# Kernel tuning notes

Measured on AMD Instinct MI355X. Metric: run time of the kernel, lower is better.

The kernel has to match this reference:

```python
import jax, jax.numpy as jnp
import numpy as np

N_ELEMENTS = 64  # StructureElementLayer(n_elements=64)


def setup_inputs() -> dict:
    key = jax.random.key(0)
    k1, k2 = jax.random.split(key)
    # x: [N, C, T, V] skeleton sequence (batch, coord channels, time, joints)
    x = jax.random.normal(k1, (256, 3, 256, 25), dtype=jnp.float32)
    # StructureElementLayer parameters (torch.rand init / ones*3 init)
    centres = jax.random.uniform(k2, (N_ELEMENTS, 2), dtype=jnp.float32)
    sharpness = jnp.ones((N_ELEMENTS, 2), dtype=jnp.float32) * 3.0
    return {"x": x, "centres": centres, "sharpness": sharpness}


def _mst_deaths(D):
    """Dim-0 Vietoris-Rips persistence deaths == MST edge weights (Prim's algorithm).

    D: [n, n] symmetric distance matrix. Returns [n-1] finite death values
    (births are all 0; the single essential (0, inf) pair contributes
    exp(-inf)=0 to the structure-element layer and is dropped).
    """
    n = D.shape[0]
    in_tree = jnp.zeros((n,), dtype=bool).at[0].set(True)
    dist = D[0]  # min distance from each node to the current tree

    def step(carry, _):
        in_tree, dist = carry
        d = jnp.where(in_tree, jnp.inf, dist)
        j = jnp.argmin(d)
        w = d[j]
        in_tree = in_tree.at[j].set(True)
        dist = jnp.minimum(dist, D[j])
        return (in_tree, dist), w

    (_, _), deaths = jax.lax.scan(step, (in_tree, dist), None, length=n - 1)
    return deaths


def _forward(x, centres, sharpness):
    xm = x.mean(1)                                  # [N, T, V]
    diff = xm[..., :, None] - xm[..., None, :]      # [N, T, V, V] pairwise joint diffs
    diff = diff.mean(-3)                            # [N, V, V]
    feat = jnp.linalg.norm(diff, axis=1)            # [N, V]  (torch.norm(., 2, dim=1))
    feat = (feat - feat.min()) / (feat.max() - feat.min())
    # Euclidean distance matrix of the N points in V-dim space (grad-safe sqrt)
    sq = jnp.sum(feat * feat, axis=1)
    D2 = sq[:, None] + sq[None, :] - 2.0 * (feat @ feat.T)
    D2 = jnp.maximum(D2, 0.0)
    D = jnp.where(D2 > 0.0, jnp.sqrt(jnp.where(D2 > 0.0, D2, 1.0)), 0.0)
    deaths = _mst_deaths(D)                         # [N-1]
    diag = jnp.stack([jnp.zeros_like(deaths), deaths], axis=-1)  # [N-1, 2] (birth, death)
    # StructureElementLayer: sum_i exp(-sum_d (p_id - c_kd)^2 * s_kd^2)
    d2 = (diag[:, None, :] - centres[None, :, :]) ** 2            # [N-1, K, 2]
    out = jnp.exp(-(d2 * (sharpness ** 2)).sum(-1)).sum(0)        # [K]
    return out


def reference(x, centres, sharpness):
    return _forward(x, centres, sharpness)
```

## Files before the change

kernel.cpp:

```cpp
#include <hip/hip_runtime.h>
#include <hip/hip_fp16.h>


#define WS_M    0
#define WS_MM   25600
#define WS_RK   28672
#define WS_DTH  29696
#define WS_NCDC 30720
#define WS_D16  65536
#define WS_MP   196608

#define INF32 0xFFFFFFFFu
#define MPSTR 132

__global__ void k_mean(const float* __restrict__ x, float* __restrict__ m,
                       unsigned int* __restrict__ Mp) {
    const int n = blockIdx.x;
    const int tid = threadIdx.x;
    if (tid < 66) Mp[n * 66 + tid] = INF32;
    __shared__ float sums[25];
    if (tid < 25) sums[tid] = 0.0f;
    __syncthreads();
    if (tid < 200) {
        const float* base = x + (long)n * 19200 + 4 * tid;
        float a0 = 0.f, a1 = 0.f, a2 = 0.f, a3 = 0.f;
        #pragma unroll
        for (int i = 0; i < 24; ++i) {
            float4 v = *reinterpret_cast<const float4*>(base + 800 * i);
            a0 += v.x; a1 += v.y; a2 += v.z; a3 += v.w;
        }
        const int v0 = (4 * tid) % 25;
        atomicAdd(&sums[v0], a0);
        atomicAdd(&sums[(v0 + 1) % 25], a1);
        atomicAdd(&sums[(v0 + 2) % 25], a2);
        atomicAdd(&sums[(v0 + 3) % 25], a3);
    }
    __syncthreads();
    if (tid < 25) m[n * 25 + tid] = sums[tid] * (1.0f / 768.0f);
}

template <int CTRL>
__device__ __forceinline__ unsigned int dpp_min_step(unsigned int v) {
    unsigned int t = (unsigned int)__builtin_amdgcn_update_dpp(
        (int)0xFFFFFFFF, (int)v, CTRL, 0xF, 0xF, false);
    return (t < v) ? t : v;
}

__global__ void __launch_bounds__(256) k_dist(const float* __restrict__ m,
                                              unsigned short* __restrict__ D16,
                                              unsigned int* __restrict__ rowKeyG,
                                              unsigned int* __restrict__ mm) {
    __shared__ float mS[6400];
    __shared__ float featS[6400];
    __shared__ unsigned int bmin, bmax;
    __shared__ unsigned int wred[4];
    const int i = blockIdx.x;
    const int t = threadIdx.x;
    if (t == 0) { bmin = 0x7F800000u; bmax = 0u; }
    #pragma unroll
    for (int it = 0; it < 7; ++it) {
        int o = it * 256 + t;
        if (o < 1600) reinterpret_cast<float4*>(mS)[o] =
            reinterpret_cast<const float4*>(m)[o];
    }
    __syncthreads();
    float r[25];
    #pragma unroll
    for (int v = 0; v < 25; ++v) r[v] = mS[t * 25 + v];
    float S1 = 0.f, S2 = 0.f;
    #pragma unroll
    for (int v = 0; v < 25; ++v) { S1 += r[v]; S2 += r[v] * r[v]; }
    float fmn = 1e30f, fmx = -1e30f;
    #pragma unroll
    for (int w = 0; w < 25; ++w) {
        float q = S2 - 2.f * r[w] * S1 + 25.f * r[w] * r[w];
        q = fmaxf(q, 0.f);
        float f = sqrtf(q);
        featS[t * 25 + w] = f;
        fmn = fminf(fmn, f); fmx = fmaxf(fmx, f);
    }
    if (i == 0) {
        atomicMin(&bmin, __float_as_uint(fmn));
        atomicMax(&bmax, __float_as_uint(fmx));
    }
    __syncthreads();
    if (i == 0 && t == 0) { mm[0] = bmin; mm[1] = bmax; }
    float fi[25];
    #pragma unroll
    for (int v = 0; v < 25; ++v) fi[v] = featS[i * 25 + v];
    float s = 0.f;
    #pragma unroll
    for (int v = 0; v < 25; ++v) { float d = fi[v] - featS[t * 25 + v]; s += d * d; }
    const unsigned int w16 = (unsigned int)__half_as_ushort(__float2half(s));
    D16[i * 256 + t] = (unsigned short)w16;
    const unsigned int lo = (i < t) ? i : t, hi = (i < t) ? t : i;
    unsigned int key = (t == i) ? INF32 : ((w16 << 16) | (lo << 8) | hi);
    key = dpp_min_step<0x111>(key);
    key = dpp_min_step<0x112>(key);
    key = dpp_min_step<0x114>(key);
    key = dpp_min_step<0x118>(key);
    key = dpp_min_step<0x142>(key);
    key = dpp_min_step<0x143>(key);
    if ((t & 63) == 63) wred[t >> 6] = key;
    __syncthreads();
    if (t == 0) {
        unsigned int b0 = wred[0] < wred[1] ? wred[0] : wred[1];
        unsigned int b1 = wred[2] < wred[3] ? wred[2] : wred[3];
        rowKeyG[i] = b0 < b1 ? b0 : b1;
    }
}

template <bool RECORD>
__device__ __forceinline__ void wave0_phase(int n, int lane,
        unsigned int* rowKeyS, unsigned char* parentS, unsigned char* newidS,
        unsigned char* cmapS, float* deaths, unsigned int* ncS, unsigned int* dcS) {
    unsigned int par[4];
    #pragma unroll
    for (int s = 0; s < 4; ++s) {
        const int i = lane + 64 * s;
        if (i < n) {
            const unsigned int rk = rowKeyS[i];
            const unsigned int u = (rk >> 8) & 0xFFu, v = rk & 0xFFu;
            unsigned int p = (u == (unsigned int)i) ? v : u;
            if (rk == INF32) p = (unsigned int)i;
            par[s] = p;
            parentS[i] = (unsigned char)p;
        }
    }
    #pragma unroll
    for (int s = 0; s < 4; ++s) {
        const int i = lane + 64 * s;
        if (i < n) {
            const unsigned int p = par[s];
            if (p != (unsigned int)i) {
                if (parentS[p] == (unsigned char)i && (unsigned int)i < p) {
                    parentS[i] = (unsigned char)i;
                } else if (RECORD) {
                    const unsigned int d = atomicAdd(dcS, 1u);
                    const unsigned int rk = rowKeyS[i];
                    deaths[d] = sqrtf(__half2float(__ushort_as_half(
                        (unsigned short)(rk >> 16))));
                }
            }
        }
    }
    for (;;) {
        bool ch = false;
        #pragma unroll
        for (int s = 0; s < 4; ++s) {
            const int i = lane + 64 * s;
            if (i < n) {
                const unsigned char p0 = parentS[i];
                const unsigned char np = parentS[p0];
                if (np != p0) { ch = true; parentS[i] = np; }
            }
        }
        if (__ballot(ch) == 0ull) break;
    }
    bool isr[4];
    #pragma unroll
    for (int s = 0; s < 4; ++s) {
        const int i = lane + 64 * s;
        isr[s] = (i < n) && (parentS[i] == (unsigned char)i);
    }
    unsigned int base = 0;
    const unsigned long long below = (1ull << lane) - 1ull;
    #pragma unroll
    for (int s = 0; s < 4; ++s) {
        const unsigned long long mask = __ballot(isr[s]);
        if (isr[s]) {
            const int i = lane + 64 * s;
            newidS[i] = (unsigned char)(base + __popcll(mask & below));
        }
        base += (unsigned int)__popcll(mask);
    }
    if (lane == 0) *ncS = base;
    #pragma unroll
    for (int s = 0; s < 4; ++s) {
        const int i = lane + 64 * s;
        if (i < n) cmapS[i] = newidS[parentS[i]];
    }
}

__global__ void __launch_bounds__(256) k_contract(const unsigned short* __restrict__ D16g,
                                                  const unsigned int* __restrict__ rowKeyG,
                                                  unsigned int* __restrict__ Mp,
                                                  float* __restrict__ deathsG,
                                                  unsigned int* __restrict__ ncdcG) {
    __shared__ unsigned int rowKeyS[256];
    __shared__ unsigned char parentS[256], newidS[256], cmapS[256];
    __shared__ unsigned int ncS, dcS;
    __shared__ float deathsS[256];
    const int tid = threadIdx.x;
    const int b = blockIdx.x;
    rowKeyS[tid] = rowKeyG[tid];
    if (tid == 0) dcS = 0;
    __syncthreads();
    if (tid < 64) {
        if (b == 0)
            wave0_phase<true>(256, tid, rowKeyS, parentS, newidS, cmapS,
                              deathsS, &ncS, &dcS);
        else
            wave0_phase<false>(256, tid, rowKeyS, parentS, newidS, cmapS,
                               nullptr, &ncS, nullptr);
    }
    __syncthreads();
    if (b == 0) {
        if (tid < dcS) deathsG[tid] = deathsS[tid];
        if (tid == 0) { ncdcG[0] = ncS; ncdcG[1] = dcS; }
    }
    const unsigned int ca = cmapS[b];
    const unsigned int cb = cmapS[tid];
    if (ca != cb) {
        const unsigned int w16 = (unsigned int)D16g[b * 256 + tid];
        const unsigned int lo = ca < cb ? ca : cb;
        const unsigned int hi = ca < cb ? cb : ca;
        atomicMin(&Mp[ca * MPSTR + cb], (w16 << 16) | (lo << 8) | hi);
    }
}

#define SA 132
#define SB 68
#define OFF_B (128 * SA)

__global__ void __launch_bounds__(1024) k_mst(const unsigned int* __restrict__ Mp,
                                              const float* __restrict__ deathsG,
                                              const unsigned int* __restrict__ ncdcG,
                                              const unsigned int* __restrict__ mm,
                                              const float* __restrict__ centres,
                                              const float* __restrict__ sharp,
                                              float* __restrict__ out) {
    __shared__ unsigned int Mb[128 * SA + 64 * SB];
    __shared__ unsigned int rowKeyS[256];
    __shared__ unsigned char parentS[256], newidS[256], cmapS[256];
    __shared__ unsigned int ncS, dcS;
    __shared__ float deaths[256];
    __shared__ float outpart[1024];
    const int tid = threadIdx.x;

    if (tid == 0) { ncS = ncdcG[0]; dcS = ncdcG[1]; }
    if (tid < 256) deaths[tid] = deathsG[tid];
    __syncthreads();
    int n = (int)ncS;

    for (int idx = tid; idx < n * SA; idx += 1024) Mb[idx] = Mp[idx];
    __syncthreads();

    int srcOff = 0, srcStr = SA, dstOff = OFF_B, dstStr = SB;
    for (int round = 0; round < 12 && n > 1; ++round) {
        if (tid < n) rowKeyS[tid] = INF32;
        __syncthreads();
        if (tid < 8 * n) {
            const int a = tid >> 3, sub = tid & 7;
            const unsigned int* row = &Mb[srcOff + a * srcStr];
            unsigned int best = INF32;
            for (int b2 = sub; b2 < n; b2 += 8) {
                const unsigned int v = row[b2];
                best = v < best ? v : best;
            }
            if (best != INF32) atomicMin(&rowKeyS[a], best);
        }
        __syncthreads();
        if (tid < 64)
            wave0_phase<true>(n, tid, rowKeyS, parentS, newidS, cmapS,
                              deaths, &ncS, &dcS);
        __syncthreads();
        const int nc = (int)ncS;
        if (nc > 1) {
            for (int w = tid; w < nc * dstStr; w += 1024) Mb[dstOff + w] = INF32;
            __syncthreads();
            if (tid < 8 * n) {
                const int a = tid >> 3, sub = tid & 7;
                const unsigned int ca = cmapS[a];
                const unsigned int* row = &Mb[srcOff + a * srcStr];
                for (int b2 = sub; b2 < n; b2 += 8) {
                    const unsigned int cb = cmapS[b2];
                    const unsigned int v = row[b2];
                    if (ca != cb && v != INF32) {
                        const unsigned int lo = ca < cb ? ca : cb;
                        const unsigned int hi = ca < cb ? cb : ca;
                        atomicMin(&Mb[dstOff + ca * dstStr + cb],
                                  (v & 0xFFFF0000u) | (lo << 8) | hi);
                    }
                }
            }
            __syncthreads();
        }
        const int t1 = srcOff; srcOff = dstOff; dstOff = t1;
        const int t2 = srcStr; srcStr = dstStr; dstStr = t2;
        n = nc;
    }

    const float mn = __uint_as_float(mm[0]);
    const float mx = __uint_as_float(mm[1]);
    const float inv = 1.0f / (mx - mn);
    const int k = tid & 63;
    const int part = tid >> 6;
    const float c0 = centres[2 * k], c1 = centres[2 * k + 1];
    const float s0 = sharp[2 * k],   s1 = sharp[2 * k + 1];
    const float t0 = c0 * c0 * s0 * s0;
    const float s1sq = s1 * s1;
    float acc = 0.f;
    for (int idx = part; idx < 255; idx += 16) {
        const float d = deaths[idx] * inv - c1;
        acc += __expf(-(t0 + d * d * s1sq));
    }
    outpart[tid] = acc;
    __syncthreads();
    if (tid < 64) {
        float s = 0.f;
        #pragma unroll
        for (int pp = 0; pp < 16; ++pp) s += outpart[tid + 64 * pp];
        out[tid] = s;
    }
}

extern "C" void kernel_launch(void* const* d_in, const int* in_sizes, int n_in,
                              void* d_out, int out_size, void* d_ws, size_t ws_size,
                              hipStream_t stream) {
    const float* x       = (const float*)d_in[0];
    const float* centres = (const float*)d_in[1];
    const float* sharp   = (const float*)d_in[2];
    float* out = (float*)d_out;
    char* ws = (char*)d_ws;
    float*          m    = (float*)(ws + WS_M);
    unsigned int*   mm   = (unsigned int*)(ws + WS_MM);
    unsigned int*   rk   = (unsigned int*)(ws + WS_RK);
    float*          dth  = (float*)(ws + WS_DTH);
    unsigned int*   ncdc = (unsigned int*)(ws + WS_NCDC);
    unsigned short* D16  = (unsigned short*)(ws + WS_D16);
    unsigned int*   Mp   = (unsigned int*)(ws + WS_MP);

    k_mean<<<256, 256, 0, stream>>>(x, m, Mp);
    k_dist<<<256, 256, 0, stream>>>(m, D16, rk, mm);
    k_contract<<<256, 256, 0, stream>>>(D16, rk, Mp, dth, ncdc);
    k_mst<<<1, 1024, 0, stream>>>(Mp, dth, ncdc, mm, centres, sharp, out);
}
```

Measured before the change: 93.14 us.

## Fold contraction into MST kernel and compute features per sample in mean kernel

Feature vectors and per-row min/max now come from the mean kernel, so every distance block no longer recomputes all 256 features redundantly. The separate contraction kernel is removed. Its first Boruvka contraction is done inside the single-block MST kernel straight from the FP16 distance matrix in shared memory, which cuts one launch and the global Mp round trip. Later Boruvka rounds run on one wave with wave barriers instead of block-wide syncs. The trade-off is that the serial single-block kernel now handles the 65K-edge contraction and the per-lane row scans on its own, with less parallelism per round.

```diff
diff --git a/kernel.cpp b/kernel.cpp
--- a/kernel.cpp
+++ b/kernel.cpp
@@ -2,24 +2,29 @@
 #include <hip/hip_fp16.h>
 
 
-#define WS_M    0
-#define WS_MM   25600
+#define WS_FEAT 0
+#define WS_FMN  26624
+#define WS_FMX  27648
 #define WS_RK   28672
-#define WS_DTH  29696
-#define WS_NCDC 30720
 #define WS_D16  65536
-#define WS_MP   196608
 
 #define INF32 0xFFFFFFFFu
-#define MPSTR 132
-
-__global__ void k_mean(const float* __restrict__ x, float* __restrict__ m,
-                       unsigned int* __restrict__ Mp) {
+#define SA 132
+#define SB 68
+#define OFF_B (128 * SA)
+
+__global__ void __launch_bounds__(256) k_feat(const float* __restrict__ x,
+                                              float* __restrict__ featG,
+                                              float* __restrict__ fmnG,
+                                              float* __restrict__ fmxG) {
+    __shared__ float sums[25];
+    __shared__ float mrow[25];
+    __shared__ float S12[2];
+    __shared__ unsigned int bmn, bmx;
     const int n = blockIdx.x;
     const int tid = threadIdx.x;
-    if (tid < 66) Mp[n * 66 + tid] = INF32;
-    __shared__ float sums[25];
     if (tid < 25) sums[tid] = 0.0f;
+    if (tid == 0) { bmn = 0x7F800000u; bmx = 0u; }
     __syncthreads();
     if (tid < 200) {
         const float* base = x + (long)n * 19200 + 4 * tid;
@@ -36,7 +41,26 @@
         atomicAdd(&sums[(v0 + 3) % 25], a3);
     }
     __syncthreads();
-    if (tid < 25) m[n * 25 + tid] = sums[tid] * (1.0f / 768.0f);
+    if (tid < 25) mrow[tid] = sums[tid] * (1.0f / 768.0f);
+    __syncthreads();
+    if (tid == 0) {
+        float S1 = 0.f, S2 = 0.f;
+        #pragma unroll
+        for (int v = 0; v < 25; ++v) { S1 += mrow[v]; S2 += mrow[v] * mrow[v]; }
+        S12[0] = S1; S12[1] = S2;
+    }
+    __syncthreads();
+    if (tid < 25) {
+        const float r = mrow[tid];
+        float q = S12[1] - 2.f * r * S12[0] + 25.f * r * r;
+        q = fmaxf(q, 0.f);
+        const float f = sqrtf(q);
+        featG[n * 26 + tid] = f;
+        atomicMin(&bmn, __float_as_uint(f));
+        atomicMax(&bmx, __float_as_uint(f));
+    }
+    __syncthreads();
+    if (tid == 0) { fmnG[n] = __uint_as_float(bmn); fmxG[n] = __uint_as_float(bmx); }
 }
 
 template <int CTRL>
@@ -46,54 +70,32 @@
     return (t < v) ? t : v;
 }
 
-__global__ void __launch_bounds__(256) k_dist(const float* __restrict__ m,
+__global__ void __launch_bounds__(256) k_dist(const float* __restrict__ featG,
                                               unsigned short* __restrict__ D16,
-                                              unsigned int* __restrict__ rowKeyG,
-                                              unsigned int* __restrict__ mm) {
-    __shared__ float mS[6400];
-    __shared__ float featS[6400];
-    __shared__ unsigned int bmin, bmax;
+                                              unsigned int* __restrict__ rowKeyG) {
+    __shared__ float featS[6656];
     __shared__ unsigned int wred[4];
     const int i = blockIdx.x;
     const int t = threadIdx.x;
-    if (t == 0) { bmin = 0x7F800000u; bmax = 0u; }
     #pragma unroll
     for (int it = 0; it < 7; ++it) {
-        int o = it * 256 + t;
-        if (o < 1600) reinterpret_cast<float4*>(mS)[o] =
-            reinterpret_cast<const float4*>(m)[o];
-    }
-    __syncthreads();
-    float r[25];
-    #pragma unroll
-    for (int v = 0; v < 25; ++v) r[v] = mS[t * 25 + v];
-    float S1 = 0.f, S2 = 0.f;
-    #pragma unroll
-    for (int v = 0; v < 25; ++v) { S1 += r[v]; S2 += r[v] * r[v]; }
-    float fmn = 1e30f, fmx = -1e30f;
-    #pragma unroll
-    for (int w = 0; w < 25; ++w) {
-        float q = S2 - 2.f * r[w] * S1 + 25.f * r[w] * r[w];
-        q = fmaxf(q, 0.f);
-        float f = sqrtf(q);
-        featS[t * 25 + w] = f;
-        fmn = fminf(fmn, f); fmx = fmaxf(fmx, f);
-    }
-    if (i == 0) {
-        atomicMin(&bmin, __float_as_uint(fmn));
-        atomicMax(&bmax, __float_as_uint(fmx));
-    }
-    __syncthreads();
-    if (i == 0 && t == 0) { mm[0] = bmin; mm[1] = bmax; }
+        const int o = it * 256 + t;
+        if (o < 1664) reinterpret_cast<float4*>(featS)[o] =
+            reinterpret_cast<const float4*>(featG)[o];
+    }
+    __syncthreads();
     float fi[25];
     #pragma unroll
-    for (int v = 0; v < 25; ++v) fi[v] = featS[i * 25 + v];
+    for (int v = 0; v < 25; ++v) fi[v] = featS[i * 26 + v];
     float s = 0.f;
     #pragma unroll
-    for (int v = 0; v < 25; ++v) { float d = fi[v] - featS[t * 25 + v]; s += d * d; }
+    for (int v = 0; v < 25; ++v) {
+        const float d = fi[v] - featS[t * 26 + v];
+        s += d * d;
+    }
     const unsigned int w16 = (unsigned int)__half_as_ushort(__float2half(s));
     D16[i * 256 + t] = (unsigned short)w16;
-    const unsigned int lo = (i < t) ? i : t, hi = (i < t) ? t : i;
+    const unsigned int lo = (t < i) ? t : i, hi = (t < i) ? i : t;
     unsigned int key = (t == i) ? INF32 : ((w16 << 16) | (lo << 8) | hi);
     key = dpp_min_step<0x111>(key);
     key = dpp_min_step<0x112>(key);
@@ -104,14 +106,14 @@
     if ((t & 63) == 63) wred[t >> 6] = key;
     __syncthreads();
     if (t == 0) {
-        unsigned int b0 = wred[0] < wred[1] ? wred[0] : wred[1];
-        unsigned int b1 = wred[2] < wred[3] ? wred[2] : wred[3];
+        const unsigned int b0 = wred[0] < wred[1] ? wred[0] : wred[1];
+        const unsigned int b1 = wred[2] < wred[3] ? wred[2] : wred[3];
         rowKeyG[i] = b0 < b1 ? b0 : b1;
     }
 }
 
 template <bool RECORD>
-__device__ __forceinline__ void wave0_phase(int n, int lane,
+__device__ __forceinline__ unsigned int wave0_phase(int n, int lane,
         unsigned int* rowKeyS, unsigned char* parentS, unsigned char* newidS,
         unsigned char* cmapS, float* deaths, unsigned int* ncS, unsigned int* dcS) {
     unsigned int par[4];
@@ -180,53 +182,13 @@
         const int i = lane + 64 * s;
         if (i < n) cmapS[i] = newidS[parentS[i]];
     }
-}
-
-__global__ void __launch_bounds__(256) k_contract(const unsigned short* __restrict__ D16g,
-                                                  const unsigned int* __restrict__ rowKeyG,
-                                                  unsigned int* __restrict__ Mp,
-                                                  float* __restrict__ deathsG,
-                                                  unsigned int* __restrict__ ncdcG) {
-    __shared__ unsigned int rowKeyS[256];
-    __shared__ unsigned char parentS[256], newidS[256], cmapS[256];
-    __shared__ unsigned int ncS, dcS;
-    __shared__ float deathsS[256];
-    const int tid = threadIdx.x;
-    const int b = blockIdx.x;
-    rowKeyS[tid] = rowKeyG[tid];
-    if (tid == 0) dcS = 0;
-    __syncthreads();
-    if (tid < 64) {
-        if (b == 0)
-            wave0_phase<true>(256, tid, rowKeyS, parentS, newidS, cmapS,
-                              deathsS, &ncS, &dcS);
-        else
-            wave0_phase<false>(256, tid, rowKeyS, parentS, newidS, cmapS,
-                               nullptr, &ncS, nullptr);
-    }
-    __syncthreads();
-    if (b == 0) {
-        if (tid < dcS) deathsG[tid] = deathsS[tid];
-        if (tid == 0) { ncdcG[0] = ncS; ncdcG[1] = dcS; }
-    }
-    const unsigned int ca = cmapS[b];
-    const unsigned int cb = cmapS[tid];
-    if (ca != cb) {
-        const unsigned int w16 = (unsigned int)D16g[b * 256 + tid];
-        const unsigned int lo = ca < cb ? ca : cb;
-        const unsigned int hi = ca < cb ? cb : ca;
-        atomicMin(&Mp[ca * MPSTR + cb], (w16 << 16) | (lo << 8) | hi);
-    }
-}
-
-#define SA 132
-#define SB 68
-#define OFF_B (128 * SA)
-
-__global__ void __launch_bounds__(1024) k_mst(const unsigned int* __restrict__ Mp,
-                                              const float* __restrict__ deathsG,
-                                              const unsigned int* __restrict__ ncdcG,
-                                              const unsigned int* __restrict__ mm,
+    return base;
+}
+
+__global__ void __launch_bounds__(1024) k_mst(const unsigned short* __restrict__ D16g,
+                                              const unsigned int* __restrict__ rowKeyG,
+                                              const float* __restrict__ fmnG,
+                                              const float* __restrict__ fmxG,
                                               const float* __restrict__ centres,
                                               const float* __restrict__ sharp,
                                               float* __restrict__ out) {
@@ -234,65 +196,103 @@
     __shared__ unsigned int rowKeyS[256];
     __shared__ unsigned char parentS[256], newidS[256], cmapS[256];
     __shared__ unsigned int ncS, dcS;
-    __shared__ float deaths[256];
+    __shared__ float deathsS[256];
+    __shared__ unsigned int mmS[2];
     __shared__ float outpart[1024];
     const int tid = threadIdx.x;
-
-    if (tid == 0) { ncS = ncdcG[0]; dcS = ncdcG[1]; }
-    if (tid < 256) deaths[tid] = deathsG[tid];
-    __syncthreads();
-    int n = (int)ncS;
-
-    for (int idx = tid; idx < n * SA; idx += 1024) Mb[idx] = Mp[idx];
-    __syncthreads();
-
-    int srcOff = 0, srcStr = SA, dstOff = OFF_B, dstStr = SB;
-    for (int round = 0; round < 12 && n > 1; ++round) {
-        if (tid < n) rowKeyS[tid] = INF32;
-        __syncthreads();
-        if (tid < 8 * n) {
-            const int a = tid >> 3, sub = tid & 7;
-            const unsigned int* row = &Mb[srcOff + a * srcStr];
-            unsigned int best = INF32;
-            for (int b2 = sub; b2 < n; b2 += 8) {
-                const unsigned int v = row[b2];
-                best = v < best ? v : best;
-            }
-            if (best != INF32) atomicMin(&rowKeyS[a], best);
-        }
-        __syncthreads();
-        if (tid < 64)
-            wave0_phase<true>(n, tid, rowKeyS, parentS, newidS, cmapS,
-                              deaths, &ncS, &dcS);
-        __syncthreads();
-        const int nc = (int)ncS;
-        if (nc > 1) {
-            for (int w = tid; w < nc * dstStr; w += 1024) Mb[dstOff + w] = INF32;
-            __syncthreads();
-            if (tid < 8 * n) {
-                const int a = tid >> 3, sub = tid & 7;
-                const unsigned int ca = cmapS[a];
+    const int wv = tid >> 6, lane = tid & 63;
+
+    if (tid < 256) rowKeyS[tid] = rowKeyG[tid];
+    if (tid == 0) { dcS = 0; mmS[0] = 0x7F800000u; mmS[1] = 0u; }
+    __syncthreads();
+
+    if (wv == 0) {
+        wave0_phase<true>(256, lane, rowKeyS, parentS, newidS, cmapS,
+                          deathsS, &ncS, &dcS);
+    } else if (wv == 15) {
+        #pragma unroll
+        for (int q = 0; q < 4; ++q) {
+            const int j = (tid - 960) * 4 + q;
+            atomicMin(&mmS[0], __float_as_uint(fmnG[j]));
+            atomicMax(&mmS[1], __float_as_uint(fmxG[j]));
+        }
+    } else {
+        for (int w = tid - 64; w < 128 * SA; w += 896) Mb[w] = INF32;
+    }
+    __syncthreads();
+
+    {
+        const unsigned int* D32 = reinterpret_cast<const unsigned int*>(D16g);
+        for (int u = tid; u < 32768; u += 1024) {
+            const unsigned int w = D32[u];
+            const int r = u >> 7;
+            const int c = (u & 127) << 1;
+            const unsigned int ca = cmapS[r];
+            const unsigned int e0 = w & 0xFFFFu;
+            const unsigned int e1 = w >> 16;
+            const unsigned int cb0 = cmapS[c];
+            const unsigned int cb1 = cmapS[c + 1];
+            if (ca != cb0) {
+                const unsigned int lo = ca < cb0 ? ca : cb0;
+                const unsigned int hi = ca < cb0 ? cb0 : ca;
+                atomicMin(&Mb[ca * SA + cb0], (e0 << 16) | (lo << 8) | hi);
+            }
+            if (ca != cb1) {
+                const unsigned int lo = ca < cb1 ? ca : cb1;
+                const unsigned int hi = ca < cb1 ? cb1 : ca;
+                atomicMin(&Mb[ca * SA + cb1], (e1 << 16) | (lo << 8) | hi);
+            }
+        }
+    }
+    __syncthreads();
+
+    if (wv == 0) {
+        int n = (int)ncS;
+        int srcOff = 0, srcStr = SA, dstOff = OFF_B, dstStr = SB;
+        for (int round = 0; round < 12 && n > 1; ++round) {
+            for (int a = lane; a < n; a += 64) {
                 const unsigned int* row = &Mb[srcOff + a * srcStr];
-                for (int b2 = sub; b2 < n; b2 += 8) {
-                    const unsigned int cb = cmapS[b2];
+                unsigned int best = INF32;
+                for (int b2 = 0; b2 < n; ++b2) {
                     const unsigned int v = row[b2];
-                    if (ca != cb && v != INF32) {
-                        const unsigned int lo = ca < cb ? ca : cb;
-                        const unsigned int hi = ca < cb ? cb : ca;
-                        atomicMin(&Mb[dstOff + ca * dstStr + cb],
-                                  (v & 0xFFFF0000u) | (lo << 8) | hi);
+                    best = v < best ? v : best;
+                }
+                rowKeyS[a] = best;
+            }
+            __builtin_amdgcn_wave_barrier();
+            const unsigned int nc = wave0_phase<true>(n, lane, rowKeyS, parentS,
+                                                      newidS, cmapS, deathsS,
+                                                      &ncS, &dcS);
+            __builtin_amdgcn_wave_barrier();
+            if (nc > 1) {
+                for (int w = lane; w < (int)nc * dstStr; w += 64)
+                    Mb[dstOff + w] = INF32;
+                __builtin_amdgcn_wave_barrier();
+                for (int a = lane; a < n; a += 64) {
+                    const unsigned int ca = cmapS[a];
+                    const unsigned int* row = &Mb[srcOff + a * srcStr];
+                    for (int b2 = 0; b2 < n; ++b2) {
+                        const unsigned int cb = cmapS[b2];
+                        const unsigned int v = row[b2];
+                        if (ca != cb && v != INF32) {
+                            const unsigned int lo = ca < cb ? ca : cb;
+                            const unsigned int hi = ca < cb ? cb : ca;
+                            atomicMin(&Mb[dstOff + ca * dstStr + cb],
+                                      (v & 0xFFFF0000u) | (lo << 8) | hi);
+                        }
                     }
                 }
-            }
-            __syncthreads();
-        }
-        const int t1 = srcOff; srcOff = dstOff; dstOff = t1;
-        const int t2 = srcStr; srcStr = dstStr; dstStr = t2;
-        n = nc;
-    }
-
-    const float mn = __uint_as_float(mm[0]);
-    const float mx = __uint_as_float(mm[1]);
+                __builtin_amdgcn_wave_barrier();
+            }
+            const int t1 = srcOff; srcOff = dstOff; dstOff = t1;
+            const int t2 = srcStr; srcStr = dstStr; dstStr = t2;
+            n = (int)nc;
+        }
+    }
+    __syncthreads();
+
+    const float mn = __uint_as_float(mmS[0]);
+    const float mx = __uint_as_float(mmS[1]);
     const float inv = 1.0f / (mx - mn);
     const int k = tid & 63;
     const int part = tid >> 6;
@@ -302,7 +302,7 @@
     const float s1sq = s1 * s1;
     float acc = 0.f;
     for (int idx = part; idx < 255; idx += 16) {
-        const float d = deaths[idx] * inv - c1;
+        const float d = deathsS[idx] * inv - c1;
         acc += __expf(-(t0 + d * d * s1sq));
     }
     outpart[tid] = acc;
@@ -323,16 +323,13 @@
     const float* sharp   = (const float*)d_in[2];
     float* out = (float*)d_out;
     char* ws = (char*)d_ws;
-    float*          m    = (float*)(ws + WS_M);
-    unsigned int*   mm   = (unsigned int*)(ws + WS_MM);
-    unsigned int*   rk   = (unsigned int*)(ws + WS_RK);
-    float*          dth  = (float*)(ws + WS_DTH);
-    unsigned int*   ncdc = (unsigned int*)(ws + WS_NCDC);
-    unsigned short* D16  = (unsigned short*)(ws + WS_D16);
-    unsigned int*   Mp   = (unsigned int*)(ws + WS_MP);
-
-    k_mean<<<256, 256, 0, stream>>>(x, m, Mp);
-    k_dist<<<256, 256, 0, stream>>>(m, D16, rk, mm);
-    k_contract<<<256, 256, 0, stream>>>(D16, rk, Mp, dth, ncdc);
-    k_mst<<<1, 1024, 0, stream>>>(Mp, dth, ncdc, mm, centres, sharp, out);
-}
+    float*          featG = (float*)(ws + WS_FEAT);
+    float*          fmnG  = (float*)(ws + WS_FMN);
+    float*          fmxG  = (float*)(ws + WS_FMX);
+    unsigned int*   rk    = (unsigned int*)(ws + WS_RK);
+    unsigned short* D16   = (unsigned short*)(ws + WS_D16);
+
+    k_feat<<<256, 256, 0, stream>>>(x, featG, fmnG, fmxG);
+    k_dist<<<256, 256, 0, stream>>>(featG, D16, rk);
+    k_mst<<<1, 1024, 0, stream>>>(D16, rk, fmnG, fmxG, centres, sharp, out);
+}
```

Result: slower. 112.5 us (+20.7%).
